# Optimization experiments

Measured on AMD Instinct MI355X. Metric: run time of the kernel, lower is better.

## Reference

```python
import jax, jax.numpy as jnp
import numpy as np


def setup_inputs() -> dict:
    key = jax.random.key(0)
    k1, k2 = jax.random.split(key)
    B, N, M = 8, 8192, 8192
    points1 = jax.random.normal(k1, (B, N, 2), dtype=jnp.float32)
    points2 = jax.random.normal(k2, (B, M, 2), dtype=jnp.float32)
    return {"points1": points1, "points2": points2}


def reference(points1, points2):
    # points1: [B, N, 2], points2: [B, M, 2]
    # Squared pairwise distances via |a|^2 + |b|^2 - 2 a.b  -> [B, N, M]
    p1_sq = jnp.sum(points1 * points1, axis=-1)  # [B, N]
    p2_sq = jnp.sum(points2 * points2, axis=-1)  # [B, M]
    cross = jnp.einsum("bnd,bmd->bnm", points1, points2)  # [B, N, M]
    sqdist = p1_sq[:, :, None] + p2_sq[:, None, :] - 2.0 * cross
    dist1 = jnp.min(sqdist, axis=2)  # [B, N]: NN of each p1 point in p2
    dist2 = jnp.min(sqdist, axis=1)  # [B, M]: NN of each p2 point in p1
    cost = jnp.mean(dist1, axis=-1) + jnp.mean(dist2, axis=-1)  # [B]
    return jnp.sum(cost)
```

## Files before the change

### kernel.cpp

```cpp
#include <hip/hip_runtime.h>


#define BATCH 8
#define NPTS  8192
#define TPB   256
#define IPT   8
#define PPB   (TPB * IPT)
#define TILES (NPTS / PPB)
#define S     32
#define JCH   (NPTS / S)
#define PARTN (2 * BATCH * S * NPTS)

__device__ inline float min3f(float a, float b, float c) {
    float d;
    asm("v_min3_f32 %0, %1, %2, %3" : "=v"(d) : "v"(a), "v"(b), "v"(c));
    return d;
}

__device__ inline float2 pkfma(float2 a, float2 b, float2 c) {
    float2 d;
    asm("v_pk_fma_f32 %0, %1, %2, %3" : "=v"(d) : "v"(a), "v"(b), "v"(c));
    return d;
}

__global__ __launch_bounds__(TPB, 4)
void chamfer_partial(const float* __restrict__ p1, const float* __restrict__ p2,
                     float* __restrict__ partial ) {
    __shared__ __align__(16) float qx[JCH];
    __shared__ __align__(16) float qy[JCH];
    __shared__ __align__(16) float qz[JCH];

    int blk   = blockIdx.x;
    int split = blk & (S - 1);      blk >>= 5;
    int tile  = blk & (TILES - 1);  blk >>= 2;
    int b     = blk & (BATCH - 1);  blk >>= 3;
    int dir   = blk;

    const float2* a  = (const float2*)(dir ? p2 : p1) + (size_t)b * NPTS;
    const float2* bp = (const float2*)(dir ? p1 : p2) + (size_t)b * NPTS + split * JCH;

    int t = threadIdx.x;

    {
        float2 v = bp[t];
        qx[t] = v.x;
        qy[t] = v.y;
        qz[t] = fmaf(v.x, v.x, v.y * v.y);
    }

    int pt_base = tile * PPB;
    float2 xp2[IPT], yp2[IPT];
    float m[IPT];
#pragma unroll
    for (int k = 0; k < IPT; ++k) {
        float2 v = a[pt_base + k * TPB + t];
        xp2[k] = make_float2(-2.0f * v.x, -2.0f * v.x);
        yp2[k] = make_float2(-2.0f * v.y, -2.0f * v.y);
        m[k]   = 3.0e38f;
    }

    __syncthreads();

    for (int j = 0; j < JCH; j += 8) {
        float4 x03 = *(const float4*)&qx[j];
        float4 x47 = *(const float4*)&qx[j + 4];
        float4 y03 = *(const float4*)&qy[j];
        float4 y47 = *(const float4*)&qy[j + 4];
        float4 z03 = *(const float4*)&qz[j];
        float4 z47 = *(const float4*)&qz[j + 4];
        float2 x01 = make_float2(x03.x, x03.y), x23 = make_float2(x03.z, x03.w);
        float2 x45 = make_float2(x47.x, x47.y), x67 = make_float2(x47.z, x47.w);
        float2 y01 = make_float2(y03.x, y03.y), y23 = make_float2(y03.z, y03.w);
        float2 y45 = make_float2(y47.x, y47.y), y67 = make_float2(y47.z, y47.w);
        float2 z01 = make_float2(z03.x, z03.y), z23 = make_float2(z03.z, z03.w);
        float2 z45 = make_float2(z47.x, z47.y), z67 = make_float2(z47.z, z47.w);
#pragma unroll
        for (int k = 0; k < IPT; ++k) {
            float2 a01 = pkfma(yp2[k], y01, pkfma(xp2[k], x01, z01));
            float2 a23 = pkfma(yp2[k], y23, pkfma(xp2[k], x23, z23));
            float2 a45 = pkfma(yp2[k], y45, pkfma(xp2[k], x45, z45));
            float2 a67 = pkfma(yp2[k], y67, pkfma(xp2[k], x67, z67));
            m[k] = min3f(m[k], a01.x, a01.y);
            m[k] = min3f(m[k], a23.x, a23.y);
            m[k] = min3f(m[k], a45.x, a45.y);
            m[k] = min3f(m[k], a67.x, a67.y);
        }
    }

    float* outp = partial + ((size_t)((dir * BATCH + b) * S + split)) * NPTS + pt_base;
#pragma unroll
    for (int k = 0; k < IPT; ++k)
        outp[k * TPB + t] = m[k];
}

__global__ __launch_bounds__(TPB)
void chamfer_reduce(const float* __restrict__ p1, const float* __restrict__ p2,
                    const float* __restrict__ partial, float* __restrict__ bsum) {
    int gid   = blockIdx.x * TPB + threadIdx.x;
    int point = gid & (NPTS - 1);
    int rest  = gid >> 13;
    int b     = rest & (BATCH - 1);
    int dir   = rest >> 3;

    const float* base = partial + ((size_t)(dir * BATCH + b) * S) * NPTS + point;
    float m = base[0];
#pragma unroll
    for (int s = 1; s < S; ++s)
        m = fminf(m, base[(size_t)s * NPTS]);

    float2 v = ((const float2*)(dir ? p2 : p1))[(size_t)b * NPTS + point];
    float d = m + fmaf(v.x, v.x, v.y * v.y);

#pragma unroll
    for (int off = 32; off > 0; off >>= 1)
        d += __shfl_down(d, off, 64);

    __shared__ float wsum[TPB / 64];
    int lane = threadIdx.x & 63;
    int w    = threadIdx.x >> 6;
    if (lane == 0) wsum[w] = d;
    __syncthreads();
    if (threadIdx.x == 0)
        bsum[blockIdx.x] = wsum[0] + wsum[1] + wsum[2] + wsum[3];
}

__global__ __launch_bounds__(TPB)
void chamfer_final(const float* __restrict__ bsum, float* __restrict__ out) {
    int t = threadIdx.x;
    float s = bsum[t] + bsum[t + TPB];

#pragma unroll
    for (int off = 32; off > 0; off >>= 1)
        s += __shfl_down(s, off, 64);

    __shared__ float wsum[TPB / 64];
    int lane = t & 63;
    int w    = t >> 6;
    if (lane == 0) wsum[w] = s;
    __syncthreads();
    if (t == 0)
        *out = (wsum[0] + wsum[1] + wsum[2] + wsum[3]) * (1.0f / NPTS);
}

extern "C" void kernel_launch(void* const* d_in, const int* in_sizes, int n_in,
                              void* d_out, int out_size, void* d_ws, size_t ws_size,
                              hipStream_t stream) {
    const float* p1 = (const float*)d_in[0];
    const float* p2 = (const float*)d_in[1];
    float* out      = (float*)d_out;
    float* partial  = (float*)d_ws;
    float* bsum     = partial + PARTN;

    chamfer_partial<<<2 * BATCH * TILES * S, TPB, 0, stream>>>(p1, p2, partial);
    chamfer_reduce<<<2 * BATCH * NPTS / TPB, TPB, 0, stream>>>(p1, p2, partial, bsum);
    chamfer_final<<<1, TPB, 0, stream>>>(bsum, out);
}
```

Measured before the change: 115.9 us.

## Feed query points as scalar SGPR operands from a precomputed SoA buffer

Adds a prep kernel that writes x, y and |p|^2 into separate SoA arrays in the workspace. The main kernel now reads these block-uniform values straight from global memory, where they can be scalar-loaded, and passes them to v_pk_fma_f32 as SGPR operands. This replaces the shared-memory staging, the LDS reads and the __syncthreads. The split count S is also halved, so each block scans a longer chunk and the partial buffer the reduce kernel reads shrinks. The cost is an extra kernel launch, plus a reliance on scalar-cache loads keeping pace with the packed FMA loop.

```diff
diff --git a/kernel.cpp b/kernel.cpp
--- a/kernel.cpp
+++ b/kernel.cpp
@@ -7,8 +7,9 @@
 #define IPT   8
 #define PPB   (TPB * IPT)
 #define TILES (NPTS / PPB)
-#define S     32
+#define S     16
 #define JCH   (NPTS / S)
+#define NARR  (2 * BATCH * NPTS)
 #define PARTN (2 * BATCH * S * NPTS)
 
 __device__ inline float min3f(float a, float b, float c) {
@@ -17,40 +18,47 @@
     return d;
 }
 
-__device__ inline float2 pkfma(float2 a, float2 b, float2 c) {
+__device__ inline float2 pkfma_vsv(float2 a, float2 b, float2 c) {
     float2 d;
-    asm("v_pk_fma_f32 %0, %1, %2, %3" : "=v"(d) : "v"(a), "v"(b), "v"(c));
+    asm("v_pk_fma_f32 %0, %1, %2, %3" : "=v"(d) : "v"(a), "s"(b), "v"(c));
     return d;
+}
+
+__global__ __launch_bounds__(TPB)
+void chamfer_prep(const float* __restrict__ p1, const float* __restrict__ p2,
+                  float* __restrict__ sx, float* __restrict__ sy,
+                  float* __restrict__ sz) {
+    int idx = blockIdx.x * TPB + threadIdx.x;
+    int arr = idx >> 16;
+    int rem = idx & (BATCH * NPTS - 1);
+    float2 v = ((const float2*)(arr ? p2 : p1))[rem];
+    sx[idx] = v.x;
+    sy[idx] = v.y;
+    sz[idx] = fmaf(v.x, v.x, v.y * v.y);
 }
 
 __global__ __launch_bounds__(TPB, 4)
 void chamfer_partial(const float* __restrict__ p1, const float* __restrict__ p2,
+                     const float* __restrict__ sx, const float* __restrict__ sy,
+                     const float* __restrict__ sz,
                      float* __restrict__ partial ) {
-    __shared__ __align__(16) float qx[JCH];
-    __shared__ __align__(16) float qy[JCH];
-    __shared__ __align__(16) float qz[JCH];
-
     int blk   = blockIdx.x;
-    int split = blk & (S - 1);      blk >>= 5;
+    int split = blk & (S - 1);      blk >>= 4;
     int tile  = blk & (TILES - 1);  blk >>= 2;
     int b     = blk & (BATCH - 1);  blk >>= 3;
     int dir   = blk;
 
-    const float2* a  = (const float2*)(dir ? p2 : p1) + (size_t)b * NPTS;
-    const float2* bp = (const float2*)(dir ? p1 : p2) + (size_t)b * NPTS + split * JCH;
+    const float2* a = (const float2*)(dir ? p2 : p1) + (size_t)b * NPTS;
+    int qoff = (1 - dir) * (BATCH * NPTS) + b * NPTS + split * JCH;
+    const float4* qx4 = (const float4*)(sx + qoff);
+    const float4* qy4 = (const float4*)(sy + qoff);
+    const float4* qz4 = (const float4*)(sz + qoff);
 
     int t = threadIdx.x;
+    int pt_base = tile * PPB;
 
-    {
-        float2 v = bp[t];
-        qx[t] = v.x;
-        qy[t] = v.y;
-        qz[t] = fmaf(v.x, v.x, v.y * v.y);
-    }
-
-    int pt_base = tile * PPB;
     float2 xp2[IPT], yp2[IPT];
-    float m[IPT];
+    float  m[IPT];
 #pragma unroll
     for (int k = 0; k < IPT; ++k) {
         float2 v = a[pt_base + k * TPB + t];
@@ -59,27 +67,22 @@
         m[k]   = 3.0e38f;
     }
 
-    __syncthreads();
-
-    for (int j = 0; j < JCH; j += 8) {
-        float4 x03 = *(const float4*)&qx[j];
-        float4 x47 = *(const float4*)&qx[j + 4];
-        float4 y03 = *(const float4*)&qy[j];
-        float4 y47 = *(const float4*)&qy[j + 4];
-        float4 z03 = *(const float4*)&qz[j];
-        float4 z47 = *(const float4*)&qz[j + 4];
-        float2 x01 = make_float2(x03.x, x03.y), x23 = make_float2(x03.z, x03.w);
-        float2 x45 = make_float2(x47.x, x47.y), x67 = make_float2(x47.z, x47.w);
-        float2 y01 = make_float2(y03.x, y03.y), y23 = make_float2(y03.z, y03.w);
-        float2 y45 = make_float2(y47.x, y47.y), y67 = make_float2(y47.z, y47.w);
+    for (int g = 0; g < JCH / 8; ++g) {
+        float4 x03 = qx4[2 * g], x47 = qx4[2 * g + 1];
+        float4 y03 = qy4[2 * g], y47 = qy4[2 * g + 1];
+        float4 z03 = qz4[2 * g], z47 = qz4[2 * g + 1];
+        float2 qx01 = make_float2(x03.x, x03.y), qx23 = make_float2(x03.z, x03.w);
+        float2 qx45 = make_float2(x47.x, x47.y), qx67 = make_float2(x47.z, x47.w);
+        float2 qy01 = make_float2(y03.x, y03.y), qy23 = make_float2(y03.z, y03.w);
+        float2 qy45 = make_float2(y47.x, y47.y), qy67 = make_float2(y47.z, y47.w);
         float2 z01 = make_float2(z03.x, z03.y), z23 = make_float2(z03.z, z03.w);
         float2 z45 = make_float2(z47.x, z47.y), z67 = make_float2(z47.z, z47.w);
 #pragma unroll
         for (int k = 0; k < IPT; ++k) {
-            float2 a01 = pkfma(yp2[k], y01, pkfma(xp2[k], x01, z01));
-            float2 a23 = pkfma(yp2[k], y23, pkfma(xp2[k], x23, z23));
-            float2 a45 = pkfma(yp2[k], y45, pkfma(xp2[k], x45, z45));
-            float2 a67 = pkfma(yp2[k], y67, pkfma(xp2[k], x67, z67));
+            float2 a01 = pkfma_vsv(yp2[k], qy01, pkfma_vsv(xp2[k], qx01, z01));
+            float2 a23 = pkfma_vsv(yp2[k], qy23, pkfma_vsv(xp2[k], qx23, z23));
+            float2 a45 = pkfma_vsv(yp2[k], qy45, pkfma_vsv(xp2[k], qx45, z45));
+            float2 a67 = pkfma_vsv(yp2[k], qy67, pkfma_vsv(xp2[k], qx67, z67));
             m[k] = min3f(m[k], a01.x, a01.y);
             m[k] = min3f(m[k], a23.x, a23.y);
             m[k] = min3f(m[k], a45.x, a45.y);
@@ -150,8 +153,12 @@
     float* out      = (float*)d_out;
     float* partial  = (float*)d_ws;
     float* bsum     = partial + PARTN;
+    float* sx       = bsum + 512;
+    float* sy       = sx + NARR;
+    float* sz       = sy + NARR;
 
-    chamfer_partial<<<2 * BATCH * TILES * S, TPB, 0, stream>>>(p1, p2, partial);
+    chamfer_prep<<<NARR / TPB, TPB, 0, stream>>>(p1, p2, sx, sy, sz);
+    chamfer_partial<<<2 * BATCH * TILES * S, TPB, 0, stream>>>(p1, p2, sx, sy, sz, partial);
     chamfer_reduce<<<2 * BATCH * NPTS / TPB, TPB, 0, stream>>>(p1, p2, partial, bsum);
     chamfer_final<<<1, TPB, 0, stream>>>(bsum, out);
 }
```

Result: slower. 120.8 us (+4.2%).

## Halve split count and fuse final reduction into reduce kernel via atomic counter

Applied to the files above, without the earlier changes.

Reduces the number of splits over the second point set from 32 to 16, so each block processes twice as many candidate points and the partial-min buffer and reduce reads shrink by half. The final sum kernel is merged into the reduce kernel using a last-block-done atomic counter, which drops one kernel launch. The counter is reset by block 0 of the partial kernel. The trade is half as many partial blocks, which lowers parallelism, and a longer serial inner loop per block.

```diff
diff --git a/kernel.cpp b/kernel.cpp
--- a/kernel.cpp
+++ b/kernel.cpp
@@ -7,9 +7,10 @@
 #define IPT   8
 #define PPB   (TPB * IPT)
 #define TILES (NPTS / PPB)
-#define S     32
+#define S     16
 #define JCH   (NPTS / S)
 #define PARTN (2 * BATCH * S * NPTS)
+#define RBLKS (2 * BATCH * NPTS / TPB)
 
 __device__ inline float min3f(float a, float b, float c) {
     float d;
@@ -25,13 +26,16 @@
 
 __global__ __launch_bounds__(TPB, 4)
 void chamfer_partial(const float* __restrict__ p1, const float* __restrict__ p2,
-                     float* __restrict__ partial ) {
+                     float* __restrict__ partial ,
+                     int* __restrict__ counter) {
     __shared__ __align__(16) float qx[JCH];
     __shared__ __align__(16) float qy[JCH];
     __shared__ __align__(16) float qz[JCH];
 
+    if (blockIdx.x == 0 && threadIdx.x == 0) *counter = 0;
+
     int blk   = blockIdx.x;
-    int split = blk & (S - 1);      blk >>= 5;
+    int split = blk & (S - 1);      blk >>= 4;
     int tile  = blk & (TILES - 1);  blk >>= 2;
     int b     = blk & (BATCH - 1);  blk >>= 3;
     int dir   = blk;
@@ -41,16 +45,16 @@
 
     int t = threadIdx.x;
 
-    {
-        float2 v = bp[t];
-        qx[t] = v.x;
-        qy[t] = v.y;
-        qz[t] = fmaf(v.x, v.x, v.y * v.y);
+    for (int j = t; j < JCH; j += TPB) {
+        float2 v = bp[j];
+        qx[j] = v.x;
+        qy[j] = v.y;
+        qz[j] = fmaf(v.x, v.x, v.y * v.y);
     }
 
     int pt_base = tile * PPB;
     float2 xp2[IPT], yp2[IPT];
-    float m[IPT];
+    float  m[IPT];
 #pragma unroll
     for (int k = 0; k < IPT; ++k) {
         float2 v = a[pt_base + k * TPB + t];
@@ -94,9 +98,15 @@
 }
 
 __global__ __launch_bounds__(TPB)
-void chamfer_reduce(const float* __restrict__ p1, const float* __restrict__ p2,
-                    const float* __restrict__ partial, float* __restrict__ bsum) {
-    int gid   = blockIdx.x * TPB + threadIdx.x;
+void chamfer_reduce_final(const float* __restrict__ p1, const float* __restrict__ p2,
+                          const float* __restrict__ partial,
+                          float* __restrict__ bsum, int* __restrict__ counter,
+                          float* __restrict__ out) {
+    __shared__ float wsum[TPB / 64];
+    __shared__ int lastflag;
+
+    int t     = threadIdx.x;
+    int gid   = blockIdx.x * TPB + t;
     int point = gid & (NPTS - 1);
     int rest  = gid >> 13;
     int b     = rest & (BATCH - 1);
@@ -115,31 +125,29 @@
     for (int off = 32; off > 0; off >>= 1)
         d += __shfl_down(d, off, 64);
 
-    __shared__ float wsum[TPB / 64];
-    int lane = threadIdx.x & 63;
-    int w    = threadIdx.x >> 6;
+    int lane = t & 63;
+    int w    = t >> 6;
     if (lane == 0) wsum[w] = d;
     __syncthreads();
-    if (threadIdx.x == 0)
+    if (t == 0) {
         bsum[blockIdx.x] = wsum[0] + wsum[1] + wsum[2] + wsum[3];
-}
+        __threadfence();
+        int n = __hip_atomic_fetch_add(counter, 1, __ATOMIC_ACQ_REL,
+                                       __HIP_MEMORY_SCOPE_AGENT);
+        lastflag = (n == RBLKS - 1);
+    }
+    __syncthreads();
 
-__global__ __launch_bounds__(TPB)
-void chamfer_final(const float* __restrict__ bsum, float* __restrict__ out) {
-    int t = threadIdx.x;
-    float s = bsum[t] + bsum[t + TPB];
-
+    if (lastflag) {
+        float s = bsum[t] + bsum[t + TPB];
 #pragma unroll
-    for (int off = 32; off > 0; off >>= 1)
-        s += __shfl_down(s, off, 64);
-
-    __shared__ float wsum[TPB / 64];
-    int lane = t & 63;
-    int w    = t >> 6;
-    if (lane == 0) wsum[w] = s;
-    __syncthreads();
-    if (t == 0)
-        *out = (wsum[0] + wsum[1] + wsum[2] + wsum[3]) * (1.0f / NPTS);
+        for (int off = 32; off > 0; off >>= 1)
+            s += __shfl_down(s, off, 64);
+        if (lane == 0) wsum[w] = s;
+        __syncthreads();
+        if (t == 0)
+            *out = (wsum[0] + wsum[1] + wsum[2] + wsum[3]) * (1.0f / NPTS);
+    }
 }
 
 extern "C" void kernel_launch(void* const* d_in, const int* in_sizes, int n_in,
@@ -150,8 +158,8 @@
     float* out      = (float*)d_out;
     float* partial  = (float*)d_ws;
     float* bsum     = partial + PARTN;
+    int*   counter  = (int*)(bsum + RBLKS);
 
-    chamfer_partial<<<2 * BATCH * TILES * S, TPB, 0, stream>>>(p1, p2, partial);
-    chamfer_reduce<<<2 * BATCH * NPTS / TPB, TPB, 0, stream>>>(p1, p2, partial, bsum);
-    chamfer_final<<<1, TPB, 0, stream>>>(bsum, out);
+    chamfer_partial<<<2 * BATCH * TILES * S, TPB, 0, stream>>>(p1, p2, partial, counter);
+    chamfer_reduce_final<<<RBLKS, TPB, 0, stream>>>(p1, p2, partial, bsum, counter, out);
 }
```

New measurement: 130.5 us. 1.13x slower.
